# Optimization experiments

Hardware: AMD Instinct MI355X
Metric: run time of the kernel (lower is better)

Reference implementation:

```python
import jax, jax.numpy as jnp
import numpy as np

ALPHA = 0.2  # leaky relu slope


def setup_inputs() -> dict:
    key = jax.random.key(0)
    k_h, k_adj, k_w, k_a = jax.random.split(key, 4)
    B, N, F_in, F_out, H = 4, 2048, 128, 64, 4
    h = jax.random.normal(k_h, (B, N, F_in), dtype=jnp.float32)
    adj = jax.random.randint(k_adj, (N, N), 0, 2).astype(jnp.float32)
    # xavier_uniform with gain=1.414 (as in reset_parameters)
    gain = 1.414
    lim_w = gain * np.sqrt(6.0 / (F_in + F_out))
    W = jax.random.uniform(k_w, (H, F_in, F_out), minval=-lim_w, maxval=lim_w, dtype=jnp.float32)
    lim_a = gain * np.sqrt(6.0 / (2 * F_out + 1))
    a = jax.random.uniform(k_a, (H, 2 * F_out, 1), minval=-lim_a, maxval=lim_a, dtype=jnp.float32)
    return {"h": h, "adj": adj, "W": W, "a": a}


def reference(h, adj, W, a):
    B, N, _ = h.shape
    F_out = W.shape[2]
    # per-head linear transform: [B, N, H, F_out]
    ht = jnp.einsum('hio,bni->bnho', W, h)
    # split attention vector into src/dst halves; a^T [h_i; h_j] = a_src.h_i + a_dst.h_j
    a_src = a[:, :F_out, 0]   # [H, F_out]
    a_dst = a[:, F_out:, 0]   # [H, F_out]
    e_src = jnp.einsum('bnho,ho->bnh', ht, a_src)  # score contribution of node i (rows)
    e_dst = jnp.einsum('bnho,ho->bnh', ht, a_dst)  # score contribution of node j (cols)
    e = e_src[:, :, None, :] + e_dst[:, None, :, :]           # [B, N, N, H]
    e = jnp.where(e >= 0, e, ALPHA * e)                        # leaky relu
    e = e + (-1e20 * (1.0 - adj))[None, :, :, None]            # adjacency mask (shared over batch/heads)
    att = jax.nn.softmax(e, axis=2)                            # softmax over neighbors j
    # dropout p=0.0 (eval-mode reference): identity
    h_prime = jnp.einsum('bmnh,bnho->bmho', att, ht)           # [B, N, H, F_out]
    return h_prime.reshape(B, N, -1)                           # concat heads -> [B, N, H*F_out]
```

## Files before the change

kernel.cpp:

```cpp
#include <hip/hip_runtime.h>

#define ALPHA 0.2f
#define LOG2E 1.44269504088896340736f

constexpr int BB  = 4;
constexpr int NN  = 2048;
constexpr int FIN = 128;
constexpr int FO  = 64;
constexpr int HH  = 4;
constexpr int CC  = BB * HH;

using half8   = __attribute__((ext_vector_type(8))) _Float16;
using floatx4 = __attribute__((ext_vector_type(4))) float;

__device__ __forceinline__ float fast_exp2(float x) {
#if __has_builtin(__builtin_amdgcn_exp2f)
  return __builtin_amdgcn_exp2f(x);
#else
  return exp2f(x);
#endif
}

union PK4 { _Float16 f[4]; uint2 u; };

__global__ __launch_bounds__(256) void gat_k12(
    const float* __restrict__ h, const float* __restrict__ W,
    const float* __restrict__ a, const float* __restrict__ adj,
    _Float16* __restrict__ htT, float* __restrict__ esrcT,
    float* __restrict__ edst, float* __restrict__ gpart,
    unsigned* __restrict__ adjbits) {
  const int blk = blockIdx.x;
  const int t = threadIdx.x;
  const int w = t >> 6, lane = t & 63;

  if (blk >= 512) {
    const int m = (blk - 512) * 4 + w;
    float areg[32];
    const float* arow = adj + (size_t)m * NN;
#pragma unroll
    for (int j = 0; j < 32; ++j) areg[j] = arow[j * 64 + lane];
#pragma unroll
    for (int j = 0; j < 32; ++j) {
      const unsigned long long mask = __ballot(areg[j] != 0.f);
      if (lane == 0) {
        adjbits[m * 64 + j * 2 + 0] = (unsigned)mask;
        adjbits[m * 64 + j * 2 + 1] = (unsigned)(mask >> 32);
      }
    }
    return;
  }

  const int c  = blk >> 5;
  const int nt = blk & 31;
  const int n0 = nt * 64;
  const int b = c >> 2, hh = c & 3;
  const int q = lane >> 4, r16 = lane & 15;

  __shared__ __align__(16) _Float16 Xs[64 * 128];
  __shared__ __align__(16) _Float16 WT[64 * 128];
  __shared__ float wasb[128];
  __shared__ float wadb[128];
  __shared__ float edsh[64];

  {
    const int k = t & 127;
    const float* wrow = W + ((size_t)hh * 128 + k) * 64;
    const float* av = a + hh * 128 + ((t >> 7) << 6);
    float s = 0.f;
#pragma unroll
    for (int o = 0; o < 16; ++o) {
      const float4 wv = *(const float4*)(wrow + o * 4);
      const float4 av4 = *(const float4*)(av + o * 4);
      s += wv.x * av4.x + wv.y * av4.y + wv.z * av4.z + wv.w * av4.w;
    }
    if (t < 128) wasb[k] = s; else wadb[k] = s;
  }

  {
    const int k = t >> 1, fh = (t & 1) * 32;
    const float* wsrc = W + ((size_t)hh * 128 + k) * 64 + fh;
    const int chunk = k >> 3, within = k & 7;
#pragma unroll
    for (int i = 0; i < 8; ++i) {
      const float4 v = *(const float4*)(wsrc + i * 4);
      const _Float16 f4[4] = {(_Float16)v.x, (_Float16)v.y,
                              (_Float16)v.z, (_Float16)v.w};
#pragma unroll
      for (int u = 0; u < 4; ++u) {
        const int f = fh + i * 4 + u;
        WT[f * 128 + ((chunk ^ (f & 15)) << 3) + within] = f4[u];
      }
    }
  }

  __syncthreads();

  {
    const int r = t >> 2, cq = t & 3;
    const float* hsrc = h + ((size_t)(b * NN + n0 + r)) * FIN + cq * 32;
    float es = 0.f, ed = 0.f;
#pragma unroll
    for (int i = 0; i < 8; ++i) {
      const float4 v = *(const float4*)(hsrc + i * 4);
      const float4 ws = *(const float4*)&wasb[cq * 32 + i * 4];
      const float4 wd = *(const float4*)&wadb[cq * 32 + i * 4];
      es += v.x * ws.x + v.y * ws.y + v.z * ws.z + v.w * ws.w;
      ed += v.x * wd.x + v.y * wd.y + v.z * wd.z + v.w * wd.w;
      PK4 pk;
      pk.f[0] = (_Float16)v.x; pk.f[1] = (_Float16)v.y;
      pk.f[2] = (_Float16)v.z; pk.f[3] = (_Float16)v.w;
      const int chunk = cq * 4 + (i >> 1);
      *(uint2*)&Xs[r * 128 + ((chunk ^ (r & 15)) << 3) + (i & 1) * 4] = pk.u;
    }
    es += __shfl_xor(es, 1, 64); es += __shfl_xor(es, 2, 64);
    ed += __shfl_xor(ed, 1, 64); ed += __shfl_xor(ed, 2, 64);
    if (cq == 0) {
      const float edl = ed * LOG2E;
      esrcT[(size_t)(n0 + r) * CC + c] = es * LOG2E;
      edst[(size_t)c * NN + n0 + r]    = edl;
      edsh[r] = edl;
    }
  }

  __syncthreads();

  if (t < 64) {
    float v = edsh[t];
#pragma unroll
    for (int off = 1; off < 64; off <<= 1) v = fmaxf(v, __shfl_xor(v, off, 64));
    if (t == 0) gpart[c * 32 + nt] = v;
  }

  floatx4 acc[4];
#pragma unroll
  for (int ft = 0; ft < 4; ++ft) acc[ft] = floatx4{0.f, 0.f, 0.f, 0.f};

  half8 afrag[4];
#pragma unroll
  for (int ks = 0; ks < 4; ++ks) {
    const int slot = (ks * 4 + q) ^ r16;
    afrag[ks] = *(const half8*)&Xs[(w * 16 + r16) * 128 + (slot << 3)];
  }
#pragma unroll
  for (int ks = 0; ks < 4; ++ks) {
#pragma unroll
    for (int ft = 0; ft < 4; ++ft) {
      const int fr = ft * 16 + r16;
      const int slot = (ks * 4 + q) ^ (fr & 15);
      const half8 bfrag = *(const half8*)&WT[fr * 128 + (slot << 3)];
      acc[ft] = __builtin_amdgcn_mfma_f32_16x16x32_f16(afrag[ks], bfrag,
                                                       acc[ft], 0, 0, 0);
    }
  }

#pragma unroll
  for (int ft = 0; ft < 4; ++ft) {
    PK4 pk;
#pragma unroll
    for (int x = 0; x < 4; ++x) pk.f[x] = (_Float16)acc[ft][x];
    const int fcol = ft * 16 + r16;
    const int n = n0 + w * 16 + q * 4;
    *(uint2*)(htT + ((size_t)c * FO + fcol) * NN + n) = pk.u;
  }
}

__global__ __launch_bounds__(1024) void gat_k3_pv(
    const _Float16* __restrict__ htT, const float* __restrict__ esrcT,
    const float* __restrict__ edst, const unsigned* __restrict__ adjbits,
    const float* __restrict__ gpart, float* __restrict__ out) {
  const int blk = blockIdx.x;
  const int c = blk >> 5;
  const int m0 = (blk & 31) * 64;
  const int b = c >> 2, hh = c & 3;
  const int t = threadIdx.x;
  const int w = t >> 6;
  const int kg = w >> 2;
  const int wl = w & 3;
  const int lane = t & 63;
  const int q = lane >> 4, r16 = lane & 15;
  const int row = m0 + wl * 16 + r16;

  __shared__ __align__(16) char smem[64512];
  _Float16* Vt = (_Float16*)smem;
  float* edsF = (float*)(smem + 32768);
  float* gmaxp = (float*)(smem + 40960);
  float* abuf = (float*)smem;

  const unsigned* abrow = adjbits + (size_t)row * 64;
  const _Float16* vsrc = htT + (size_t)c * FO * NN;

  const int f0 = t >> 4, sg0 = t & 15;
  const size_t goff0 = (size_t)f0 * NN + (size_t)((sg0 ^ (f0 & 15)) * 8);

#define STAGE(BUF, NBASE)                                                      \
  __builtin_amdgcn_global_load_lds(                                            \
      (const __attribute__((address_space(1))) void*)(vsrc + goff0 + (NBASE)), \
      (__attribute__((address_space(3))) void*)(smem + (BUF)*16384 + t*16),    \
      16, 0, 0)

  STAGE(0, 0);

  *(float2*)&edsF[t * 2] = *(const float2*)(edst + (size_t)c * NN + t * 2);
  {
    float gv = (t < 32) ? gpart[c * 32 + t] : -3.0e38f;
    if (t < 64) {
#pragma unroll
      for (int off = 1; off < 32; off <<= 1)
        gv = fmaxf(gv, __shfl_xor(gv, off, 64));
      if (t == 0) *gmaxp = gv;
    }
  }
  __syncthreads();

  const float em = esrcT[(size_t)row * CC + c];
  const float gm = *gmaxp;
  const float s0 = em + gm;
  const float rm = (s0 >= 0.f) ? s0 : ALPHA * s0;
  const float em1 = em - rm;
  const float em2 = fmaf(ALPHA, em, -rm);

  floatx4 acc[4];
#pragma unroll
  for (int ft = 0; ft < 4; ++ft) acc[ft] = floatx4{0.f, 0.f, 0.f, 0.f};
  floatx4 accs = floatx4{0.f, 0.f, 0.f, 0.f};

  half8 ones;
#pragma unroll
  for (int k = 0; k < 8; ++k) ones[k] = (_Float16)1.0f;

  for (int step = 0; step < 16; ++step) {
    const int n0k = step * 128 + kg * 32;
    half8 afrag;
    const unsigned bits = abrow[step * 4 + kg] >> (q * 8);
    const float4 ea = *(const float4*)&edsF[n0k + q * 8];
    const float4 eb = *(const float4*)&edsF[n0k + q * 8 + 4];
    const float xs[8] = {ea.x, ea.y, ea.z, ea.w, eb.x, eb.y, eb.z, eb.w};
#pragma unroll
    for (int k = 0; k < 8; ++k) {
      const float t1 = em1 + xs[k];
      const float t2 = fmaf(ALPHA, xs[k], em2);
      float tt = fmaxf(t1, t2);
      tt = ((bits >> k) & 1u) ? tt : -3.0e38f;
      afrag[k] = (_Float16)fast_exp2(tt);
    }
    __syncthreads();
    if (step + 1 < 16) STAGE((step + 1) & 1, (step + 1) * 128);
    const int bufo = (step & 1) * 8192;
    accs = __builtin_amdgcn_mfma_f32_16x16x32_f16(afrag, ones, accs, 0, 0, 0);
#pragma unroll
    for (int ft = 0; ft < 4; ++ft) {
      const int fr = ft * 16 + r16;
      const int oct = kg * 4 + q;
      const half8 bfrag =
          *(const half8*)&Vt[bufo + fr * 128 + ((oct ^ (fr & 15)) << 3)];
      acc[ft] = __builtin_amdgcn_mfma_f32_16x16x32_f16(afrag, bfrag,
                                                       acc[ft], 0, 0, 0);
    }
  }

  __syncthreads();
  if (kg >= 1) {
    const int base = ((kg - 1) * 256 + (t & 255)) * 21;
#pragma unroll
    for (int ft = 0; ft < 4; ++ft)
#pragma unroll
      for (int x = 0; x < 4; ++x) abuf[base + ft * 4 + x] = acc[ft][x];
#pragma unroll
    for (int x = 0; x < 4; ++x) abuf[base + 16 + x] = accs[x];
  }
  __syncthreads();
  if (kg == 0) {
#pragma unroll
    for (int g = 0; g < 3; ++g) {
      const int base = (g * 256 + t) * 21;
#pragma unroll
      for (int ft = 0; ft < 4; ++ft)
#pragma unroll
        for (int x = 0; x < 4; ++x) acc[ft][x] += abuf[base + ft * 4 + x];
#pragma unroll
      for (int x = 0; x < 4; ++x) accs[x] += abuf[base + 16 + x];
    }
#pragma unroll
    for (int x = 0; x < 4; ++x) {
      const float rinv = 1.0f / accs[x];
      const int mrow = m0 + wl * 16 + q * 4 + x;
      float* op = out + ((size_t)b * NN + mrow) * 256 + hh * 64;
#pragma unroll
      for (int ft = 0; ft < 4; ++ft) op[ft * 16 + r16] = acc[ft][x] * rinv;
    }
  }
#undef STAGE
}

extern "C" void kernel_launch(void* const* d_in, const int* in_sizes, int n_in,
                              void* d_out, int out_size, void* d_ws, size_t ws_size,
                              hipStream_t stream) {
  const float* h   = (const float*)d_in[0];
  const float* adj = (const float*)d_in[1];
  const float* W   = (const float*)d_in[2];
  const float* a   = (const float*)d_in[3];
  float* out = (float*)d_out;

  char* ws = (char*)d_ws;
  _Float16* htT   = (_Float16*)(ws);
  float* esrcT    = (float*)(ws + 4 * 1024 * 1024);
  float* edst     = (float*)(ws + 4 * 1024 * 1024 + 131072);
  unsigned* abits = (unsigned*)(ws + 4 * 1024 * 1024 + 2 * 131072);
  float* gpart    = (float*)(ws + 4 * 1024 * 1024 + 2 * 131072 + 524288);

  gat_k12<<<dim3(1024), dim3(256), 0, stream>>>(h, W, a, adj, htT, esrcT,
                                                edst, gpart, abits);
  gat_k3_pv<<<dim3(CC * (NN / 64)), dim3(1024), 0, stream>>>(htT, esrcT, edst,
                                                             abits, gpart, out);
}
```

Before: 112.1 us.

## Double K-step size in PV loop, remap block order, reorder k12 blocks

```diff
diff --git a/kernel.cpp b/kernel.cpp
--- a/kernel.cpp
+++ b/kernel.cpp
@@ -33,8 +33,8 @@
   const int t = threadIdx.x;
   const int w = t >> 6, lane = t & 63;
 
-  if (blk >= 512) {
-    const int m = (blk - 512) * 4 + w;
+  if (blk < 512) {
+    const int m = blk * 4 + w;
     float areg[32];
     const float* arow = adj + (size_t)m * NN;
 #pragma unroll
@@ -50,8 +50,9 @@
     return;
   }
 
-  const int c  = blk >> 5;
-  const int nt = blk & 31;
+  const int pb = blk - 512;
+  const int c  = (pb & 7) | (((pb >> 3) & 1) << 3);
+  const int nt = pb >> 4;
   const int n0 = nt * 64;
   const int b = c >> 2, hh = c & 3;
   const int q = lane >> 4, r16 = lane & 15;
@@ -164,13 +165,13 @@
   }
 }
 
-__global__ __launch_bounds__(1024) void gat_k3_pv(
+__global__ __launch_bounds__(1024, 8) void gat_k3_pv(
     const _Float16* __restrict__ htT, const float* __restrict__ esrcT,
     const float* __restrict__ edst, const unsigned* __restrict__ adjbits,
     const float* __restrict__ gpart, float* __restrict__ out) {
-  const int blk = blockIdx.x;
-  const int c = blk >> 5;
-  const int m0 = (blk & 31) * 64;
+  const int blk0 = blockIdx.x;
+  const int c  = (blk0 & 7) | (((blk0 >> 3) & 1) << 3);
+  const int m0 = (blk0 >> 4) * 64;
   const int b = c >> 2, hh = c & 3;
   const int t = threadIdx.x;
   const int w = t >> 6;
@@ -180,23 +181,31 @@
   const int q = lane >> 4, r16 = lane & 15;
   const int row = m0 + wl * 16 + r16;
 
-  __shared__ __align__(16) char smem[64512];
+  __shared__ __align__(16) char smem[73744];
   _Float16* Vt = (_Float16*)smem;
-  float* edsF = (float*)(smem + 32768);
-  float* gmaxp = (float*)(smem + 40960);
+  float* edsF = (float*)(smem + 65536);
+  float* gmaxp = (float*)(smem + 73728);
   float* abuf = (float*)smem;
 
   const unsigned* abrow = adjbits + (size_t)row * 64;
   const _Float16* vsrc = htT + (size_t)c * FO * NN;
 
-  const int f0 = t >> 4, sg0 = t & 15;
-  const size_t goff0 = (size_t)f0 * NN + (size_t)((sg0 ^ (f0 & 15)) * 8);
+  const int f0 = t >> 5, sg0 = t & 31;
+  const int f1 = (t + 1024) >> 5;
+  const size_t goff0 = (size_t)f0 * NN + (size_t)((sg0 ^ (f0 & 31)) * 8);
+  const size_t goff1 = (size_t)f1 * NN + (size_t)((sg0 ^ (f1 & 31)) * 8);
 
 #define STAGE(BUF, NBASE)                                                      \
-  __builtin_amdgcn_global_load_lds(                                            \
-      (const __attribute__((address_space(1))) void*)(vsrc + goff0 + (NBASE)), \
-      (__attribute__((address_space(3))) void*)(smem + (BUF)*16384 + t*16),    \
-      16, 0, 0)
+  do {                                                                         \
+    __builtin_amdgcn_global_load_lds(                                          \
+        (const __attribute__((address_space(1))) void*)(vsrc + goff0 + (NBASE)),\
+        (__attribute__((address_space(3))) void*)(smem + (BUF)*32768 + t*16),  \
+        16, 0, 0);                                                             \
+    __builtin_amdgcn_global_load_lds(                                          \
+        (const __attribute__((address_space(1))) void*)(vsrc + goff1 + (NBASE)),\
+        (__attribute__((address_space(3))) void*)(smem + (BUF)*32768 + (t+1024)*16),\
+        16, 0, 0);                                                             \
+  } while (0)
 
   STAGE(0, 0);
 
@@ -228,32 +237,52 @@
 #pragma unroll
   for (int k = 0; k < 8; ++k) ones[k] = (_Float16)1.0f;
 
-  for (int step = 0; step < 16; ++step) {
-    const int n0k = step * 128 + kg * 32;
-    half8 afrag;
-    const unsigned bits = abrow[step * 4 + kg] >> (q * 8);
-    const float4 ea = *(const float4*)&edsF[n0k + q * 8];
-    const float4 eb = *(const float4*)&edsF[n0k + q * 8 + 4];
-    const float xs[8] = {ea.x, ea.y, ea.z, ea.w, eb.x, eb.y, eb.z, eb.w};
-#pragma unroll
-    for (int k = 0; k < 8; ++k) {
-      const float t1 = em1 + xs[k];
-      const float t2 = fmaf(ALPHA, xs[k], em2);
-      float tt = fmaxf(t1, t2);
-      tt = ((bits >> k) & 1u) ? tt : -3.0e38f;
-      afrag[k] = (_Float16)fast_exp2(tt);
-    }
+  for (int step = 0; step < 8; ++step) {
+    const int nbase = step * 256 + kg * 64;
+    const uint2 bw = *(const uint2*)&abrow[step * 8 + kg * 2];
+
+    half8 afrag0, afrag1;
+#pragma unroll
+    for (int h2 = 0; h2 < 2; ++h2) {
+      const int nb = nbase + h2 * 32 + q * 8;
+      const float4 ea = *(const float4*)&edsF[nb];
+      const float4 eb = *(const float4*)&edsF[nb + 4];
+      const float xs[8] = {ea.x, ea.y, ea.z, ea.w, eb.x, eb.y, eb.z, eb.w};
+      const unsigned bits = ((h2 == 0) ? bw.x : bw.y) >> (q * 8);
+      half8 af;
+#pragma unroll
+      for (int k = 0; k < 8; ++k) {
+        const float t1 = em1 + xs[k];
+        const float t2 = fmaf(ALPHA, xs[k], em2);
+        float tt = fmaxf(t1, t2);
+        tt = ((bits >> k) & 1u) ? tt : -3.0e38f;
+        af[k] = (_Float16)fast_exp2(tt);
+      }
+      if (h2 == 0) afrag0 = af; else afrag1 = af;
+    }
+
     __syncthreads();
-    if (step + 1 < 16) STAGE((step + 1) & 1, (step + 1) * 128);
-    const int bufo = (step & 1) * 8192;
-    accs = __builtin_amdgcn_mfma_f32_16x16x32_f16(afrag, ones, accs, 0, 0, 0);
+    if (step + 1 < 8) STAGE((step + 1) & 1, (step + 1) * 256);
+
+    const int bufo = (step & 1) * 16384;
+    accs = __builtin_amdgcn_mfma_f32_16x16x32_f16(afrag0, ones, accs, 0, 0, 0);
 #pragma unroll
     for (int ft = 0; ft < 4; ++ft) {
       const int fr = ft * 16 + r16;
-      const int oct = kg * 4 + q;
+      const int oct = kg * 8 + q;
       const half8 bfrag =
-          *(const half8*)&Vt[bufo + fr * 128 + ((oct ^ (fr & 15)) << 3)];
-      acc[ft] = __builtin_amdgcn_mfma_f32_16x16x32_f16(afrag, bfrag,
+          *(const half8*)&Vt[bufo + fr * 256 + ((oct ^ (fr & 31)) << 3)];
+      acc[ft] = __builtin_amdgcn_mfma_f32_16x16x32_f16(afrag0, bfrag,
+                                                       acc[ft], 0, 0, 0);
+    }
+    accs = __builtin_amdgcn_mfma_f32_16x16x32_f16(afrag1, ones, accs, 0, 0, 0);
+#pragma unroll
+    for (int ft = 0; ft < 4; ++ft) {
+      const int fr = ft * 16 + r16;
+      const int oct = kg * 8 + 4 + q;
+      const half8 bfrag =
+          *(const half8*)&Vt[bufo + fr * 256 + ((oct ^ (fr & 31)) << 3)];
+      acc[ft] = __builtin_amdgcn_mfma_f32_16x16x32_f16(afrag1, bfrag,
                                                        acc[ft], 0, 0, 0);
     }
   }
```

New measurement: 113.7 us. Within noise of the previous version (+1.5%).

## Triple-buffer V staging with manual waitcnt, stage adjacency bits in LDS, remap blocks

Applied to the files above, without the earlier changes.

```diff
diff --git a/kernel.cpp b/kernel.cpp
--- a/kernel.cpp
+++ b/kernel.cpp
@@ -33,8 +33,8 @@
   const int t = threadIdx.x;
   const int w = t >> 6, lane = t & 63;
 
-  if (blk >= 512) {
-    const int m = (blk - 512) * 4 + w;
+  if (blk < 512) {
+    const int m = blk * 4 + w;
     float areg[32];
     const float* arow = adj + (size_t)m * NN;
 #pragma unroll
@@ -50,8 +50,9 @@
     return;
   }
 
-  const int c  = blk >> 5;
-  const int nt = blk & 31;
+  const int pb = blk - 512;
+  const int c  = (pb & 7) | (((pb >> 3) & 1) << 3);
+  const int nt = pb >> 4;
   const int n0 = nt * 64;
   const int b = c >> 2, hh = c & 3;
   const int q = lane >> 4, r16 = lane & 15;
@@ -164,13 +165,13 @@
   }
 }
 
-__global__ __launch_bounds__(1024) void gat_k3_pv(
+__global__ __launch_bounds__(1024, 8) void gat_k3_pv(
     const _Float16* __restrict__ htT, const float* __restrict__ esrcT,
     const float* __restrict__ edst, const unsigned* __restrict__ adjbits,
     const float* __restrict__ gpart, float* __restrict__ out) {
-  const int blk = blockIdx.x;
-  const int c = blk >> 5;
-  const int m0 = (blk & 31) * 64;
+  const int blk0 = blockIdx.x;
+  const int c  = (blk0 & 7) | (((blk0 >> 3) & 1) << 3);
+  const int m0 = (blk0 >> 4) * 64;
   const int b = c >> 2, hh = c & 3;
   const int t = threadIdx.x;
   const int w = t >> 6;
@@ -179,14 +180,15 @@
   const int lane = t & 63;
   const int q = lane >> 4, r16 = lane & 15;
   const int row = m0 + wl * 16 + r16;
-
-  __shared__ __align__(16) char smem[64512];
-  _Float16* Vt = (_Float16*)smem;
-  float* edsF = (float*)(smem + 32768);
-  float* gmaxp = (float*)(smem + 40960);
-  float* abuf = (float*)smem;
-
-  const unsigned* abrow = adjbits + (size_t)row * 64;
+  const int rl  = wl * 16 + r16;
+
+  __shared__ __align__(16) char smem[73744];
+  _Float16* Vt   = (_Float16*)smem;
+  float* edsF    = (float*)(smem + 49152);
+  unsigned* abL  = (unsigned*)(smem + 57344);
+  float* gmaxp   = (float*)(smem + 73728);
+  float* abuf    = (float*)smem;
+
   const _Float16* vsrc = htT + (size_t)c * FO * NN;
 
   const int f0 = t >> 4, sg0 = t & 15;
@@ -198,21 +200,22 @@
       (__attribute__((address_space(3))) void*)(smem + (BUF)*16384 + t*16),    \
       16, 0, 0)
 
-  STAGE(0, 0);
-
-  *(float2*)&edsF[t * 2] = *(const float2*)(edst + (size_t)c * NN + t * 2);
-  {
-    float gv = (t < 32) ? gpart[c * 32 + t] : -3.0e38f;
-    if (t < 64) {
-#pragma unroll
-      for (int off = 1; off < 32; off <<= 1)
-        gv = fmaxf(gv, __shfl_xor(gv, off, 64));
-      if (t == 0) *gmaxp = gv;
-    }
-  }
-  __syncthreads();
-
   const float em = esrcT[(size_t)row * CC + c];
+  const float2 edv = *(const float2*)(edst + (size_t)c * NN + t * 2);
+  const uint4 abv = *(const uint4*)&adjbits[(size_t)(m0 + (t >> 4)) * 64 +
+                                            (t & 15) * 4];
+  float gv = (t < 32) ? gpart[c * 32 + t] : -3.0e38f;
+
+  *(float2*)&edsF[t * 2] = edv;
+  *(uint4*)&abL[(t >> 4) * 64 + (t & 15) * 4] = abv;
+  if (t < 64) {
+#pragma unroll
+    for (int off = 1; off < 32; off <<= 1)
+      gv = fmaxf(gv, __shfl_xor(gv, off, 64));
+    if (t == 0) *gmaxp = gv;
+  }
+  __syncthreads();
+
   const float gm = *gmaxp;
   const float s0 = em + gm;
   const float rm = (s0 >= 0.f) ? s0 : ALPHA * s0;
@@ -228,13 +231,18 @@
 #pragma unroll
   for (int k = 0; k < 8; ++k) ones[k] = (_Float16)1.0f;
 
+  STAGE(0, 0);
+  STAGE(1, 128);
+
+#pragma unroll
   for (int step = 0; step < 16; ++step) {
-    const int n0k = step * 128 + kg * 32;
+    const int bufs = step % 3;
+    const unsigned bits = abL[rl * 64 + step * 4 + kg] >> (q * 8);
+    const int nb = step * 128 + kg * 32 + q * 8;
+    const float4 ea = *(const float4*)&edsF[nb];
+    const float4 eb = *(const float4*)&edsF[nb + 4];
+    const float xs[8] = {ea.x, ea.y, ea.z, ea.w, eb.x, eb.y, eb.z, eb.w};
     half8 afrag;
-    const unsigned bits = abrow[step * 4 + kg] >> (q * 8);
-    const float4 ea = *(const float4*)&edsF[n0k + q * 8];
-    const float4 eb = *(const float4*)&edsF[n0k + q * 8 + 4];
-    const float xs[8] = {ea.x, ea.y, ea.z, ea.w, eb.x, eb.y, eb.z, eb.w};
 #pragma unroll
     for (int k = 0; k < 8; ++k) {
       const float t1 = em1 + xs[k];
@@ -243,9 +251,18 @@
       tt = ((bits >> k) & 1u) ? tt : -3.0e38f;
       afrag[k] = (_Float16)fast_exp2(tt);
     }
-    __syncthreads();
-    if (step + 1 < 16) STAGE((step + 1) & 1, (step + 1) * 128);
-    const int bufo = (step & 1) * 8192;
+
+    if (step < 15) {
+      asm volatile("s_waitcnt vmcnt(1) lgkmcnt(0)" ::: "memory");
+    } else {
+      asm volatile("s_waitcnt vmcnt(0) lgkmcnt(0)" ::: "memory");
+    }
+    __builtin_amdgcn_s_barrier();
+    asm volatile("" ::: "memory");
+
+    if (step <= 13) STAGE((step + 2) % 3, (step + 2) * 128);
+
+    const int bufo = bufs * 8192;
     accs = __builtin_amdgcn_mfma_f32_16x16x32_f16(afrag, ones, accs, 0, 0, 0);
 #pragma unroll
     for (int ft = 0; ft < 4; ++ft) {
```

After: 110.4 us. No clear change (-1.5%).
